# Kernel optimization log

Hardware: AMD Instinct MI355X
Metric: run time of the kernel (lower is better)

The kernel has to match this reference:

```python
import jax, jax.numpy as jnp
import numpy as np

V, E, H, B, S = 50257, 512, 512, 64, 2048


def setup_inputs() -> dict:
    key = jax.random.key(0)
    ks = jax.random.split(key, 12)
    w = lambda k, shape: jax.random.normal(k, shape, dtype=jnp.float32) * 0.02
    return {
        "input_seq": jax.random.randint(ks[0], (1, B), 0, V),
        "last_hidden": jax.random.normal(ks[1], (1, B, H), dtype=jnp.float32),
        "encoder_outputs": jax.random.normal(ks[2], (S, B, H), dtype=jnp.float32),
        "emb": w(ks[3], (V, E)),
        "w_ih": w(ks[4], (3 * H, E)),
        "w_hh": w(ks[5], (3 * H, H)),
        "b_ih": jnp.zeros((3 * H,), jnp.float32),
        "b_hh": jnp.zeros((3 * H,), jnp.float32),
        "w_concat": w(ks[6], (H, 2 * H)),
        "b_concat": jnp.zeros((H,), jnp.float32),
        "w_out": w(ks[7], (V, H)),
        "b_out": jnp.zeros((V,), jnp.float32),
    }


def gru_step(x, h, w_ih, w_hh, b_ih, b_hh):
    # PyTorch GRU cell: gates ordered [r, z, n]
    gi = x @ w_ih.T + b_ih  # [B, 3H]
    gh = h @ w_hh.T + b_hh  # [B, 3H]
    i_r, i_z, i_n = jnp.split(gi, 3, axis=1)
    h_r, h_z, h_n = jnp.split(gh, 3, axis=1)
    r = jax.nn.sigmoid(i_r + h_r)
    z = jax.nn.sigmoid(i_z + h_z)
    n = jnp.tanh(i_n + r * h_n)
    return (1.0 - z) * n + z * h


def reference(input_seq, last_hidden, encoder_outputs, emb, w_ih, w_hh,
              b_ih, b_hh, w_concat, b_concat, w_out, b_out):
    x = emb[input_seq[0]]            # [B, E] embedding lookup (seq len 1)
    h = last_hidden[0]               # [B, H]
    h_new = gru_step(x, h, w_ih, w_hh, b_ih, b_hh)  # [B, H]
    hidden = h_new[None]             # [1, B, H]
    rnn_output = h_new               # [B, H]
    # 'dot' attention: energies[b, s] = <rnn_output[b], encoder_outputs[s, b]>
    energies = jnp.einsum('bh,sbh->bs', rnn_output, encoder_outputs)
    attn = jax.nn.softmax(energies, axis=1)          # [B, S]
    context = jnp.einsum('bs,sbh->bh', attn, encoder_outputs)  # [B, H]
    concat_output = jnp.tanh(
        jnp.concatenate([rnn_output, context], axis=1) @ w_concat.T + b_concat)
    output = concat_output @ w_out.T + b_out         # [B, V]
    return output, hidden, attn[:, None, :]
```

## Files before the change

### kernel.cpp

```cpp
#include <hip/hip_runtime.h>
#include <math.h>

#define NB 64
#define NS 2048
#define NH 512
#define NE 512
#define NV 50257
#define H3 1536
#define KSL 8
#define NCH 32

typedef __attribute__((ext_vector_type(8))) short bf16x8;
typedef __attribute__((ext_vector_type(4))) float f32x4;

#define GI_OFF    0
#define GH_OFF    (GI_OFF + KSL*H3*NB)
#define HNEW_OFF  (GH_OFF + KSL*H3*NB)
#define EN_OFF    (HNEW_OFF + NB*NH)
#define PCTX_OFF  (EN_OFF + NB*NS)
#define PM_OFF    (PCTX_OFF + NB*NCH*NH)
#define PL_OFF    (PM_OFF + NB*NCH)
#define CPART_OFF (PL_OFF + NB*NCH)
#define CTX_OFF   (CPART_OFF + 4*NH*NB)
#define CCB_OFF   (CTX_OFF + NB*NH)

#define HID_OFF  ((size_t)NB*NV)
#define ATTN_OFF (HID_OFF + (size_t)NB*NH)

__device__ __forceinline__ unsigned short f2bf(float f) {
    unsigned u = __builtin_bit_cast(unsigned, f);
    u += 0x7FFFu + ((u >> 16) & 1u);
    return (unsigned short)(u >> 16);
}

__global__ __launch_bounds__(256) void k1_gru_gemm(
    const int* __restrict__ seq, const float* __restrict__ lh,
    const float* __restrict__ emb, const float* __restrict__ wih,
    const float* __restrict__ whh, float* __restrict__ ws)
{
    __shared__ float xl[64][65];
    __shared__ float hl[64][65];
    __shared__ int idxl[64];
    const int t = threadIdx.x;
    const int b = t & 63;
    const int j0 = __builtin_amdgcn_readfirstlane(blockIdx.x * 16 + (t >> 6) * 4);
    const int k0 = blockIdx.y * 64;
    if (t < 64) idxl[t] = seq[t];
    __syncthreads();
    {
        const int r = t >> 2;
        const int c = (t & 3) * 16;
        #pragma unroll
        for (int q = 0; q < 4; ++q) {
            const float4 xv = *(const float4*)&emb[(size_t)idxl[r] * NE + k0 + c + q*4];
            const float4 hv = *(const float4*)&lh[r * NH + k0 + c + q*4];
            xl[r][c+q*4+0]=xv.x; xl[r][c+q*4+1]=xv.y; xl[r][c+q*4+2]=xv.z; xl[r][c+q*4+3]=xv.w;
            hl[r][c+q*4+0]=hv.x; hl[r][c+q*4+1]=hv.y; hl[r][c+q*4+2]=hv.z; hl[r][c+q*4+3]=hv.w;
        }
    }
    __syncthreads();
    float ai[4] = {0.f,0.f,0.f,0.f};
    float ah[4] = {0.f,0.f,0.f,0.f};
    #pragma unroll 4
    for (int e = 0; e < 64; e += 4) {
        const float x0=xl[b][e], x1=xl[b][e+1], x2=xl[b][e+2], x3=xl[b][e+3];
        const float h0=hl[b][e], h1=hl[b][e+1], h2=hl[b][e+2], h3=hl[b][e+3];
        #pragma unroll
        for (int jj = 0; jj < 4; ++jj) {
            const float4 wi = *(const float4*)&wih[(size_t)(j0+jj)*NE + k0 + e];
            const float4 wh = *(const float4*)&whh[(size_t)(j0+jj)*NH + k0 + e];
            ai[jj] = fmaf(x0,wi.x, fmaf(x1,wi.y, fmaf(x2,wi.z, fmaf(x3,wi.w, ai[jj]))));
            ah[jj] = fmaf(h0,wh.x, fmaf(h1,wh.y, fmaf(h2,wh.z, fmaf(h3,wh.w, ah[jj]))));
        }
    }
    float* gi = ws + GI_OFF + (size_t)blockIdx.y * H3 * NB;
    float* gh = ws + GH_OFF + (size_t)blockIdx.y * H3 * NB;
    #pragma unroll
    for (int jj = 0; jj < 4; ++jj) {
        gi[(j0+jj)*NB + b] = ai[jj];
        gh[(j0+jj)*NB + b] = ah[jj];
    }
}

__global__ __launch_bounds__(256) void k2_gates(
    const float* __restrict__ lh, const float* __restrict__ bih,
    const float* __restrict__ bhh, float* __restrict__ ws, float* __restrict__ out)
{
    const int gid = blockIdx.x * 256 + threadIdx.x;
    const int b = gid & 63;
    const int h = gid >> 6;
    const float* gi = ws + GI_OFF;
    const float* gh = ws + GH_OFF;
    const int P = H3 * NB;
    float ir = bih[h], iz = bih[512+h], inn = bih[1024+h];
    float hr = bhh[h], hz = bhh[512+h], hnn = bhh[1024+h];
    #pragma unroll
    for (int s = 0; s < KSL; ++s) {
        ir  += gi[s*P + h*NB + b];
        iz  += gi[s*P + (512+h)*NB + b];
        inn += gi[s*P + (1024+h)*NB + b];
        hr  += gh[s*P + h*NB + b];
        hz  += gh[s*P + (512+h)*NB + b];
        hnn += gh[s*P + (1024+h)*NB + b];
    }
    const float r = 1.f / (1.f + __expf(-(ir + hr)));
    const float z = 1.f / (1.f + __expf(-(iz + hz)));
    const float nx = inn + r * hnn;
    const float e2 = __expf(-2.f * fabsf(nx));
    const float n = copysignf((1.f - e2) / (1.f + e2), nx);
    const float hnew = (1.f - z) * n + z * lh[b*NH + h];
    ws[HNEW_OFF + b*NH + h] = hnew;
    out[HID_OFF + (size_t)b*NH + h] = hnew;
}

__global__ __launch_bounds__(256) void k3_attn(
    const float* __restrict__ enc, float* __restrict__ ws)
{
    const int t = threadIdx.x;
    const int w = t >> 6;
    const int l = t & 63;
    const int b = blockIdx.x >> 5;
    const int chunk = blockIdx.x & 31;
    const float* hn = ws + HNEW_OFF + b * NH;
    const float4 hq0 = *(const float4*)&hn[l*4];
    const float4 hq1 = *(const float4*)&hn[256 + l*4];
    const int s0 = chunk * 64 + w * 16;
    const float* rowb = enc + ((size_t)s0 * NB + b) * NH;
    float m = -INFINITY, lsum = 0.f;
    float cx[8] = {0.f,0.f,0.f,0.f,0.f,0.f,0.f,0.f};
    float ekeep = 0.f;
    f32x4 a0 = __builtin_nontemporal_load((const f32x4*)&rowb[l*4]);
    f32x4 a1 = __builtin_nontemporal_load((const f32x4*)&rowb[256 + l*4]);
    for (int i = 0; i < 16; ++i) {
        const f32x4 r0 = a0, r1 = a1;
        if (i < 15) {
            const float* nr = rowb + (size_t)(i+1) * NB * NH;
            a0 = __builtin_nontemporal_load((const f32x4*)&nr[l*4]);
            a1 = __builtin_nontemporal_load((const f32x4*)&nr[256 + l*4]);
        }
        float d = r0.x*hq0.x;
        d = fmaf(r0.y,hq0.y,d); d = fmaf(r0.z,hq0.z,d); d = fmaf(r0.w,hq0.w,d);
        d = fmaf(r1.x,hq1.x,d); d = fmaf(r1.y,hq1.y,d); d = fmaf(r1.z,hq1.z,d); d = fmaf(r1.w,hq1.w,d);
        d += __shfl_xor(d, 32);
        d += __shfl_xor(d, 16);
        d += __shfl_xor(d, 8);
        d += __shfl_xor(d, 4);
        d += __shfl_xor(d, 2);
        d += __shfl_xor(d, 1);
        if (l == i) ekeep = d;
        const float mn = fmaxf(m, d);
        if (mn > m) {
            const float sc = __expf(m - mn);
            lsum *= sc;
            #pragma unroll
            for (int k = 0; k < 8; ++k) cx[k] *= sc;
            m = mn;
        }
        const float p = __expf(d - m);
        lsum += p;
        cx[0]=fmaf(p,r0.x,cx[0]); cx[1]=fmaf(p,r0.y,cx[1]);
        cx[2]=fmaf(p,r0.z,cx[2]); cx[3]=fmaf(p,r0.w,cx[3]);
        cx[4]=fmaf(p,r1.x,cx[4]); cx[5]=fmaf(p,r1.y,cx[5]);
        cx[6]=fmaf(p,r1.z,cx[6]); cx[7]=fmaf(p,r1.w,cx[7]);
    }
    if (l < 16) ws[EN_OFF + (size_t)b * NS + s0 + l] = ekeep;
    __shared__ float ctxl[4][NH];
    __shared__ float ml[4], ll[4];
    #pragma unroll
    for (int k = 0; k < 4; ++k) {
        ctxl[w][l*4+k]       = cx[k];
        ctxl[w][256 + l*4+k] = cx[4+k];
    }
    if (l == 0) { ml[w] = m; ll[w] = lsum; }
    __syncthreads();
    const float M = fmaxf(fmaxf(ml[0], ml[1]), fmaxf(ml[2], ml[3]));
    const float w0 = __expf(ml[0]-M), w1 = __expf(ml[1]-M);
    const float w2 = __expf(ml[2]-M), w3 = __expf(ml[3]-M);
    for (int e = t; e < NH; e += 256) {
        const float c = ctxl[0][e]*w0 + ctxl[1][e]*w1 + ctxl[2][e]*w2 + ctxl[3][e]*w3;
        ws[PCTX_OFF + ((size_t)b*NCH + chunk)*NH + e] = c;
    }
    if (t == 0) {
        ws[PM_OFF + b*NCH + chunk] = M;
        ws[PL_OFF + b*NCH + chunk] = ll[0]*w0 + ll[1]*w1 + ll[2]*w2 + ll[3]*w3;
    }
}

__global__ __launch_bounds__(256) void k4_combine(
    float* __restrict__ ws, float* __restrict__ out)
{
    const int b = blockIdx.x;
    const int t = threadIdx.x;
    float pm[NCH], pw[NCH];
    float M = -INFINITY;
    #pragma unroll
    for (int c = 0; c < NCH; ++c) { pm[c] = ws[PM_OFF + b*NCH + c]; M = fmaxf(M, pm[c]); }
    float L = 0.f;
    #pragma unroll
    for (int c = 0; c < NCH; ++c) { pw[c] = __expf(pm[c] - M); L += ws[PL_OFF + b*NCH + c] * pw[c]; }
    const float invL = 1.f / L;
    for (int e = t; e < NH; e += 256) {
        float acc = 0.f;
        #pragma unroll
        for (int c = 0; c < NCH; ++c)
            acc += ws[PCTX_OFF + ((size_t)b*NCH + c)*NH + e] * pw[c];
        ws[CTX_OFF + b*NH + e] = acc * invL;
    }
    for (int s = t; s < NS; s += 256)
        out[ATTN_OFF + (size_t)b*NS + s] = __expf(ws[EN_OFF + (size_t)b*NS + s] - M) * invL;
}

__global__ __launch_bounds__(256) void k5_concat_gemm(
    const float* __restrict__ wcat, float* __restrict__ ws)
{
    __shared__ float al[64][65];
    const int t = threadIdx.x;
    const int b = t & 63;
    const int j0 = __builtin_amdgcn_readfirstlane(blockIdx.x * 16 + (t >> 6) * 4);
    const int kc = blockIdx.y;
    const float* A = ws + ((kc < 2) ? HNEW_OFF : CTX_OFF);
    const int kb = (kc & 1) * 256;
    float acc[4] = {0.f,0.f,0.f,0.f};
    const int c4 = (t & 15) * 4;
    const int r0 = t >> 4;
    for (int ch = 0; ch < 4; ++ch) {
        const int k0 = kb + ch * 64;
        __syncthreads();
        #pragma unroll
        for (int i = 0; i < 4; ++i) {
            const int r = r0 + i * 16;
            const float4 v = *(const float4*)&A[r * NH + k0 + c4];
            al[r][c4+0]=v.x; al[r][c4+1]=v.y; al[r][c4+2]=v.z; al[r][c4+3]=v.w;
        }
        __syncthreads();
        #pragma unroll 4
        for (int e = 0; e < 64; e += 4) {
            const float a0v=al[b][e], a1v=al[b][e+1], a2v=al[b][e+2], a3v=al[b][e+3];
            #pragma unroll
            for (int jj = 0; jj < 4; ++jj) {
                const float4 wq = *(const float4*)&wcat[(size_t)(j0+jj)*1024 + kc*256 + ch*64 + e];
                acc[jj] = fmaf(a0v,wq.x, fmaf(a1v,wq.y, fmaf(a2v,wq.z, fmaf(a3v,wq.w, acc[jj]))));
            }
        }
    }
    #pragma unroll
    for (int jj = 0; jj < 4; ++jj)
        ws[CPART_OFF + ((size_t)kc*NH + j0+jj)*NB + b] = acc[jj];
}

__global__ __launch_bounds__(256) void k5b_concat_fin(
    const float* __restrict__ bcat, float* __restrict__ ws)
{
    const int t = threadIdx.x;
    const int b = t & 63;
    const int j = blockIdx.x * 4 + (t >> 6);
    float v = bcat[j];
    #pragma unroll
    for (int kc = 0; kc < 4; ++kc)
        v += ws[CPART_OFF + ((size_t)kc*NH + j)*NB + b];
    const float e2 = __expf(-2.f * fabsf(v));
    const float th = copysignf((1.f - e2) / (1.f + e2), v);
    unsigned short* ccb = (unsigned short*)(ws + CCB_OFF);
    ccb[b*NH + j] = f2bf(th);
}

__global__ __launch_bounds__(128) void k6_mfma(
    const float* __restrict__ wout, const float* __restrict__ bout,
    const unsigned short* __restrict__ ccb, float* __restrict__ out)
{
    const int t = threadIdx.x;
    const int w = t >> 6;
    const int l = t & 63;
    const int lm = l & 15;
    const int kg = l >> 4;
    const int j = blockIdx.x * 32 + w * 16 + lm;
    const int jc = j < NV ? j : NV - 1;
    const float* wrow = wout + (size_t)jc * NH + kg * 8;
    f32x4 acc0 = {0.f,0.f,0.f,0.f};
    f32x4 acc1 = {0.f,0.f,0.f,0.f};
    f32x4 acc2 = {0.f,0.f,0.f,0.f};
    f32x4 acc3 = {0.f,0.f,0.f,0.f};
    #pragma unroll 4
    for (int ks = 0; ks < 16; ++ks) {
        const float4 w0 = *(const float4*)(wrow + ks * 32);
        const float4 w1 = *(const float4*)(wrow + ks * 32 + 4);
        bf16x8 bf;
        bf[0] = (short)f2bf(w0.x); bf[1] = (short)f2bf(w0.y);
        bf[2] = (short)f2bf(w0.z); bf[3] = (short)f2bf(w0.w);
        bf[4] = (short)f2bf(w1.x); bf[5] = (short)f2bf(w1.y);
        bf[6] = (short)f2bf(w1.z); bf[7] = (short)f2bf(w1.w);
        const int ka = ks * 32 + kg * 8;
        const bf16x8 a0 = *(const bf16x8*)&ccb[(0*16 + lm) * NH + ka];
        const bf16x8 a1 = *(const bf16x8*)&ccb[(1*16 + lm) * NH + ka];
        const bf16x8 a2 = *(const bf16x8*)&ccb[(2*16 + lm) * NH + ka];
        const bf16x8 a3 = *(const bf16x8*)&ccb[(3*16 + lm) * NH + ka];
        acc0 = __builtin_amdgcn_mfma_f32_16x16x32_bf16(a0, bf, acc0, 0, 0, 0);
        acc1 = __builtin_amdgcn_mfma_f32_16x16x32_bf16(a1, bf, acc1, 0, 0, 0);
        acc2 = __builtin_amdgcn_mfma_f32_16x16x32_bf16(a2, bf, acc2, 0, 0, 0);
        acc3 = __builtin_amdgcn_mfma_f32_16x16x32_bf16(a3, bf, acc3, 0, 0, 0);
    }
    if (j < NV) {
        const float bj = bout[jc];
        #pragma unroll
        for (int r = 0; r < 4; ++r) {
            out[(size_t)(0*16 + kg*4 + r) * NV + j] = acc0[r] + bj;
            out[(size_t)(1*16 + kg*4 + r) * NV + j] = acc1[r] + bj;
            out[(size_t)(2*16 + kg*4 + r) * NV + j] = acc2[r] + bj;
            out[(size_t)(3*16 + kg*4 + r) * NV + j] = acc3[r] + bj;
        }
    }
}

extern "C" void kernel_launch(void* const* d_in, const int* in_sizes, int n_in,
                              void* d_out, int out_size, void* d_ws, size_t ws_size,
                              hipStream_t stream) {
    (void)in_sizes; (void)n_in; (void)out_size; (void)ws_size;
    const int*   seq  = (const int*)  d_in[0];
    const float* lh   = (const float*)d_in[1];
    const float* enc  = (const float*)d_in[2];
    const float* emb  = (const float*)d_in[3];
    const float* wih  = (const float*)d_in[4];
    const float* whh  = (const float*)d_in[5];
    const float* bih  = (const float*)d_in[6];
    const float* bhh  = (const float*)d_in[7];
    const float* wcat = (const float*)d_in[8];
    const float* bcat = (const float*)d_in[9];
    const float* wout = (const float*)d_in[10];
    const float* bout = (const float*)d_in[11];
    float* out = (float*)d_out;
    float* ws  = (float*)d_ws;

    k1_gru_gemm <<<dim3(96, KSL), 256, 0, stream>>>(seq, lh, emb, wih, whh, ws);
    k2_gates    <<<128, 256, 0, stream>>>(lh, bih, bhh, ws, out);
    k3_attn     <<<2048, 256, 0, stream>>>(enc, ws);
    k4_combine  <<<64, 256, 0, stream>>>(ws, out);
    k5_concat_gemm<<<dim3(32, 4), 256, 0, stream>>>(wcat, ws);
    k5b_concat_fin<<<128, 256, 0, stream>>>(bcat, ws);
    k6_mfma     <<<1571, 128, 0, stream>>>(wout, bout,
                     (const unsigned short*)(ws + CCB_OFF), out);
}
```

Before: 132.8 us.

## Fuse concat GEMM with tanh epilogue, split combine over slices, use packed bf16 convert

```diff
diff --git a/kernel.cpp b/kernel.cpp
--- a/kernel.cpp
+++ b/kernel.cpp
@@ -20,8 +20,7 @@
 #define PCTX_OFF  (EN_OFF + NB*NS)
 #define PM_OFF    (PCTX_OFF + NB*NCH*NH)
 #define PL_OFF    (PM_OFF + NB*NCH)
-#define CPART_OFF (PL_OFF + NB*NCH)
-#define CTX_OFF   (CPART_OFF + 4*NH*NB)
+#define CTX_OFF   (PL_OFF + NB*NCH)
 #define CCB_OFF   (CTX_OFF + NB*NH)
 
 #define HID_OFF  ((size_t)NB*NV)
@@ -190,78 +189,74 @@
     float* __restrict__ ws, float* __restrict__ out)
 {
     const int b = blockIdx.x;
-    const int t = threadIdx.x;
-    float pm[NCH], pw[NCH];
+    const int sl = blockIdx.y;
+    const int t = threadIdx.x;
+    __shared__ float pml[NCH], pll[NCH], pwl[NCH];
+    if (t < NCH) { pml[t] = ws[PM_OFF + b*NCH + t]; pll[t] = ws[PL_OFF + b*NCH + t]; }
+    __syncthreads();
     float M = -INFINITY;
     #pragma unroll
-    for (int c = 0; c < NCH; ++c) { pm[c] = ws[PM_OFF + b*NCH + c]; M = fmaxf(M, pm[c]); }
+    for (int c = 0; c < NCH; ++c) M = fmaxf(M, pml[c]);
+    if (t < NCH) pwl[t] = __expf(pml[t] - M);
+    __syncthreads();
     float L = 0.f;
     #pragma unroll
-    for (int c = 0; c < NCH; ++c) { pw[c] = __expf(pm[c] - M); L += ws[PL_OFF + b*NCH + c] * pw[c]; }
+    for (int c = 0; c < NCH; ++c) L += pll[c] * pwl[c];
     const float invL = 1.f / L;
-    for (int e = t; e < NH; e += 256) {
+    const int e = sl * 128 + (t & 127);
+    if (t < 128) {
         float acc = 0.f;
-        #pragma unroll
+        #pragma unroll 8
         for (int c = 0; c < NCH; ++c)
-            acc += ws[PCTX_OFF + ((size_t)b*NCH + c)*NH + e] * pw[c];
+            acc += ws[PCTX_OFF + ((size_t)b*NCH + c)*NH + e] * pwl[c];
         ws[CTX_OFF + b*NH + e] = acc * invL;
     }
-    for (int s = t; s < NS; s += 256)
+    for (int s = sl * 512 + t; s < sl * 512 + 512; s += 256)
         out[ATTN_OFF + (size_t)b*NS + s] = __expf(ws[EN_OFF + (size_t)b*NS + s] - M) * invL;
 }
 
-__global__ __launch_bounds__(256) void k5_concat_gemm(
-    const float* __restrict__ wcat, float* __restrict__ ws)
+__global__ __launch_bounds__(256) void kC_concat(
+    const float* __restrict__ wcat, const float* __restrict__ bcat,
+    float* __restrict__ ws)
 {
     __shared__ float al[64][65];
     const int t = threadIdx.x;
     const int b = t & 63;
-    const int j0 = __builtin_amdgcn_readfirstlane(blockIdx.x * 16 + (t >> 6) * 4);
-    const int kc = blockIdx.y;
-    const float* A = ws + ((kc < 2) ? HNEW_OFF : CTX_OFF);
-    const int kb = (kc & 1) * 256;
-    float acc[4] = {0.f,0.f,0.f,0.f};
-    const int c4 = (t & 15) * 4;
-    const int r0 = t >> 4;
-    for (int ch = 0; ch < 4; ++ch) {
-        const int k0 = kb + ch * 64;
+    const int j0 = __builtin_amdgcn_readfirstlane(blockIdx.x * 8 + (t >> 6) * 2);
+    float acc0 = 0.f, acc1 = 0.f;
+    for (int ch = 0; ch < 16; ++ch) {
+        const float* A = ws + ((ch < 8) ? (HNEW_OFF + ch*64) : (CTX_OFF + (ch-8)*64));
         __syncthreads();
-        #pragma unroll
-        for (int i = 0; i < 4; ++i) {
-            const int r = r0 + i * 16;
-            const float4 v = *(const float4*)&A[r * NH + k0 + c4];
-            al[r][c4+0]=v.x; al[r][c4+1]=v.y; al[r][c4+2]=v.z; al[r][c4+3]=v.w;
+        {
+            const int r = t >> 2;
+            const int c = (t & 3) * 16;
+            #pragma unroll
+            for (int q = 0; q < 4; ++q) {
+                const float4 v = *(const float4*)&A[r * NH + c + q*4];
+                al[r][c+q*4+0]=v.x; al[r][c+q*4+1]=v.y; al[r][c+q*4+2]=v.z; al[r][c+q*4+3]=v.w;
+            }
         }
         __syncthreads();
         #pragma unroll 4
         for (int e = 0; e < 64; e += 4) {
-            const float a0v=al[b][e], a1v=al[b][e+1], a2v=al[b][e+2], a3v=al[b][e+3];
-            #pragma unroll
-            for (int jj = 0; jj < 4; ++jj) {
-                const float4 wq = *(const float4*)&wcat[(size_t)(j0+jj)*1024 + kc*256 + ch*64 + e];
-                acc[jj] = fmaf(a0v,wq.x, fmaf(a1v,wq.y, fmaf(a2v,wq.z, fmaf(a3v,wq.w, acc[jj]))));
-            }
-        }
-    }
-    #pragma unroll
-    for (int jj = 0; jj < 4; ++jj)
-        ws[CPART_OFF + ((size_t)kc*NH + j0+jj)*NB + b] = acc[jj];
-}
-
-__global__ __launch_bounds__(256) void k5b_concat_fin(
-    const float* __restrict__ bcat, float* __restrict__ ws)
-{
-    const int t = threadIdx.x;
-    const int b = t & 63;
-    const int j = blockIdx.x * 4 + (t >> 6);
-    float v = bcat[j];
-    #pragma unroll
-    for (int kc = 0; kc < 4; ++kc)
-        v += ws[CPART_OFF + ((size_t)kc*NH + j)*NB + b];
-    const float e2 = __expf(-2.f * fabsf(v));
-    const float th = copysignf((1.f - e2) / (1.f + e2), v);
+            const float x0=al[b][e], x1=al[b][e+1], x2=al[b][e+2], x3=al[b][e+3];
+            const float4 q0 = *(const float4*)&wcat[(size_t)j0*1024 + ch*64 + e];
+            const float4 q1 = *(const float4*)&wcat[(size_t)(j0+1)*1024 + ch*64 + e];
+            acc0 = fmaf(x0,q0.x, fmaf(x1,q0.y, fmaf(x2,q0.z, fmaf(x3,q0.w, acc0))));
+            acc1 = fmaf(x0,q1.x, fmaf(x1,q1.y, fmaf(x2,q1.z, fmaf(x3,q1.w, acc1))));
+        }
+    }
     unsigned short* ccb = (unsigned short*)(ws + CCB_OFF);
-    ccb[b*NH + j] = f2bf(th);
+    {
+        const float v = acc0 + bcat[j0];
+        const float e2 = __expf(-2.f * fabsf(v));
+        ccb[b*NH + j0] = f2bf(copysignf((1.f - e2) / (1.f + e2), v));
+    }
+    {
+        const float v = acc1 + bcat[j0+1];
+        const float e2 = __expf(-2.f * fabsf(v));
+        ccb[b*NH + j0+1] = f2bf(copysignf((1.f - e2) / (1.f + e2), v));
+    }
 }
 
 __global__ __launch_bounds__(128) void k6_mfma(
@@ -284,20 +279,20 @@
     for (int ks = 0; ks < 16; ++ks) {
         const float4 w0 = *(const float4*)(wrow + ks * 32);
         const float4 w1 = *(const float4*)(wrow + ks * 32 + 4);
-        bf16x8 bf;
-        bf[0] = (short)f2bf(w0.x); bf[1] = (short)f2bf(w0.y);
-        bf[2] = (short)f2bf(w0.z); bf[3] = (short)f2bf(w0.w);
-        bf[4] = (short)f2bf(w1.x); bf[5] = (short)f2bf(w1.y);
-        bf[6] = (short)f2bf(w1.z); bf[7] = (short)f2bf(w1.w);
+        union { bf16x8 v; unsigned u[4]; } bb;
+        asm("v_cvt_pk_bf16_f32 %0, %1, %2" : "=v"(bb.u[0]) : "v"(w0.x), "v"(w0.y));
+        asm("v_cvt_pk_bf16_f32 %0, %1, %2" : "=v"(bb.u[1]) : "v"(w0.z), "v"(w0.w));
+        asm("v_cvt_pk_bf16_f32 %0, %1, %2" : "=v"(bb.u[2]) : "v"(w1.x), "v"(w1.y));
+        asm("v_cvt_pk_bf16_f32 %0, %1, %2" : "=v"(bb.u[3]) : "v"(w1.z), "v"(w1.w));
         const int ka = ks * 32 + kg * 8;
         const bf16x8 a0 = *(const bf16x8*)&ccb[(0*16 + lm) * NH + ka];
         const bf16x8 a1 = *(const bf16x8*)&ccb[(1*16 + lm) * NH + ka];
         const bf16x8 a2 = *(const bf16x8*)&ccb[(2*16 + lm) * NH + ka];
         const bf16x8 a3 = *(const bf16x8*)&ccb[(3*16 + lm) * NH + ka];
-        acc0 = __builtin_amdgcn_mfma_f32_16x16x32_bf16(a0, bf, acc0, 0, 0, 0);
-        acc1 = __builtin_amdgcn_mfma_f32_16x16x32_bf16(a1, bf, acc1, 0, 0, 0);
-        acc2 = __builtin_amdgcn_mfma_f32_16x16x32_bf16(a2, bf, acc2, 0, 0, 0);
-        acc3 = __builtin_amdgcn_mfma_f32_16x16x32_bf16(a3, bf, acc3, 0, 0, 0);
+        acc0 = __builtin_amdgcn_mfma_f32_16x16x32_bf16(a0, bb.v, acc0, 0, 0, 0);
+        acc1 = __builtin_amdgcn_mfma_f32_16x16x32_bf16(a1, bb.v, acc1, 0, 0, 0);
+        acc2 = __builtin_amdgcn_mfma_f32_16x16x32_bf16(a2, bb.v, acc2, 0, 0, 0);
+        acc3 = __builtin_amdgcn_mfma_f32_16x16x32_bf16(a3, bb.v, acc3, 0, 0, 0);
     }
     if (j < NV) {
         const float bj = bout[jc];
@@ -333,9 +328,8 @@
     k1_gru_gemm <<<dim3(96, KSL), 256, 0, stream>>>(seq, lh, emb, wih, whh, ws);
     k2_gates    <<<128, 256, 0, stream>>>(lh, bih, bhh, ws, out);
     k3_attn     <<<2048, 256, 0, stream>>>(enc, ws);
-    k4_combine  <<<64, 256, 0, stream>>>(ws, out);
-    k5_concat_gemm<<<dim3(32, 4), 256, 0, stream>>>(wcat, ws);
-    k5b_concat_fin<<<128, 256, 0, stream>>>(bcat, ws);
+    k4_combine  <<<dim3(64, 4), 256, 0, stream>>>(ws, out);
+    kC_concat   <<<64, 256, 0, stream>>>(wcat, bcat, ws);
     k6_mfma     <<<1571, 128, 0, stream>>>(wout, bout,
                      (const unsigned short*)(ws + CCB_OFF), out);
 }
```

Measured after the change: 145.3 us. 9.4% more time.
